# Performance work log

Measured on AMD Instinct MI355X. Metric: run time of the kernel, lower is better.

## Reference

```python
import jax, jax.numpy as jnp
import numpy as np
import math

B, N, E, H = 2, 2048, 1024, 16
D = E // H

def setup_inputs() -> dict:
    key = jax.random.key(0)
    ks = jax.random.split(key, 9)
    s = 1.0 / math.sqrt(E)
    return {
        "x": jax.random.normal(ks[0], (B, N, E), dtype=jnp.float32),
        "Wq": jax.random.uniform(ks[1], (E, E), jnp.float32, -s, s),
        "bq": jax.random.uniform(ks[2], (E,), jnp.float32, -s, s),
        "Wk": jax.random.uniform(ks[3], (E, E), jnp.float32, -s, s),
        "bk": jax.random.uniform(ks[4], (E,), jnp.float32, -s, s),
        "Wv": jax.random.uniform(ks[5], (E, E), jnp.float32, -s, s),
        "bv": jax.random.uniform(ks[6], (E,), jnp.float32, -s, s),
        "Wo": jax.random.uniform(ks[7], (E, E), jnp.float32, -s, s),
        "bo": jax.random.uniform(ks[8], (E,), jnp.float32, -s, s),
    }

def _split_heads(t):
    # [b, n, (h d)] -> [b, h, n, d]
    b, n, _ = t.shape
    return t.reshape(b, n, H, D).transpose(0, 2, 1, 3)

def reference(x, Wq, bq, Wk, bk, Wv, bv, Wo, bo):
    q = _split_heads(x @ Wq.T + bq)
    k = _split_heads(x @ Wk.T + bk)
    v = _split_heads(x @ Wv.T + bv)
    energy = jnp.einsum('bhqd,bhkd->bhqk', q, k)
    # Faithful to source: softmax first, THEN divide by sqrt(n_embedding)
    attention = jax.nn.softmax(energy, axis=-1) / jnp.sqrt(jnp.float32(E))
    out = jnp.einsum('bhqk,bhkd->bhqd', attention, v)
    out = out.transpose(0, 2, 1, 3).reshape(x.shape[0], x.shape[1], E)
    return out @ Wo.T + bo
```

## Files before the change

### kernel.cpp

```cpp
#include <hip/hip_runtime.h>


typedef __bf16 bf16x8 __attribute__((ext_vector_type(8)));
typedef float  f32x4  __attribute__((ext_vector_type(4)));
typedef float  f32x16 __attribute__((ext_vector_type(16)));
using u16 = unsigned short;
using u32 = unsigned int;
typedef u16 u16x8 __attribute__((ext_vector_type(8)));
typedef u16 u16x4 __attribute__((ext_vector_type(4)));
typedef u32 u32x4 __attribute__((ext_vector_type(4)));

constexpr int BATCH = 2, SEQ = 2048, EMB = 1024, NH = 16, HD = 64;
constexpr int MTOT = BATCH * SEQ;
constexpr int KTOT = EMB;
constexpr int NTOT = EMB;
constexpr float LOG2E = 1.44269504088896340736f;

constexpr size_t OFF_XBF = 0;
constexpr size_t OFF_WQ  = 8u * 1024 * 1024;
constexpr size_t OFF_WK  = OFF_WQ + 2u * 1024 * 1024;
constexpr size_t OFF_WV  = OFF_WK + 2u * 1024 * 1024;
constexpr size_t OFF_WO  = OFF_WV + 2u * 1024 * 1024;
constexpr size_t OFF_Q   = OFF_WO + 2u * 1024 * 1024;
constexpr size_t OFF_K   = OFF_Q  + 8u * 1024 * 1024;
constexpr size_t OFF_VT  = OFF_K  + 8u * 1024 * 1024;

__device__ __forceinline__ u16 f2bf(float f) {
  u32 u = __builtin_bit_cast(u32, f);
  u = (u + 0x7fffu + ((u >> 16) & 1u)) >> 16;
  return (u16)u;
}

__device__ __forceinline__ bf16x8 ld_bf16x8(const u16* p) {
  return __builtin_bit_cast(bf16x8, *(const u16x8*)p);
}

__device__ __forceinline__ float fexp2(float x) {
#if __has_builtin(__builtin_amdgcn_exp2f)
  return __builtin_amdgcn_exp2f(x);
#else
  return exp2f(x);
#endif
}

__device__ __forceinline__ float fmax3(float a, float b, float c) {
  float d;
  asm("v_max3_f32 %0, %1, %2, %3" : "=v"(d) : "v"(a), "v"(b), "v"(c));
  return d;
}

__device__ __forceinline__ u32 cvtpk(float lo, float hi_) {
  u32 r;
  asm("v_cvt_pk_bf16_f32 %0, %1, %2" : "=v"(r) : "v"(lo), "v"(hi_));
  return r;
}

__device__ __forceinline__ void stage16(const void* g, void* l) {
#if __has_builtin(__builtin_amdgcn_global_load_lds)
  __builtin_amdgcn_global_load_lds(
      (__attribute__((address_space(1))) void*)const_cast<void*>(g),
      (__attribute__((address_space(3))) void*)l, 16, 0, 0);
#else
  int lane = threadIdx.x & 63;
  uint4 v = *(const uint4*)g;
  *(uint4*)((char*)l + lane * 16) = v;
#endif
}

__global__ __launch_bounds__(256) void cvt_all(
    const float* __restrict__ x, const float* __restrict__ wq,
    const float* __restrict__ wk, const float* __restrict__ wv,
    const float* __restrict__ wo, u16* __restrict__ ox, u16* __restrict__ oq,
    u16* __restrict__ okk, u16* __restrict__ ov, u16* __restrict__ oo) {
  int id = blockIdx.x;
  const float* in;
  u16* out;
  int i;
  if (id < 4096) {
    in = x; out = ox; i = id * 256 + threadIdx.x;
  } else {
    int z = (id - 4096) >> 10, r = (id - 4096) & 1023;
    in = (z == 0) ? wq : (z == 1) ? wk : (z == 2) ? wv : wo;
    out = (z == 0) ? oq : (z == 1) ? okk : (z == 2) ? ov : oo;
    i = r * 256 + threadIdx.x;
  }
  float4 f = ((const float4*)in)[i];
  u32 lo = (u32)f2bf(f.x) | ((u32)f2bf(f.y) << 16);
  u32 hi = (u32)f2bf(f.z) | ((u32)f2bf(f.w) << 16);
  ((uint2*)out)[i] = make_uint2(lo, hi);
}

__device__ __forceinline__ void gemm_bt_core(const u16* __restrict__ A,
                                             const u16* __restrict__ Bm,
                                             const float* __restrict__ bias,
                                             void* __restrict__ out, int mode,
                                             float oscale) {
  __shared__ __align__(16) u16 smem[2][2][128 * 32];
  const int tid = threadIdx.x, w = tid >> 6, ln = tid & 63;
  const int wr = w >> 1, wc = w & 1, qq = ln >> 4, t = ln & 15;
  const int m0 = blockIdx.y * 128, n0 = blockIdx.x * 128;

  f32x4 acc[4][4] = {};

#define GSTAGE(bi, kt)                                                         \
  {                                                                            \
    _Pragma("unroll") for (int j = 0; j < 2; j++) {                            \
      int ck = w * 128 + j * 64 + ln;                                          \
      int r = ck >> 2, c2 = ck & 3;                                            \
      stage16(&A[(size_t)(m0 + r) * KTOT + (kt) + c2 * 8],                     \
              &smem[bi][0][(w * 128 + j * 64) * 8]);                           \
      stage16(&Bm[(size_t)(n0 + r) * KTOT + (kt) + c2 * 8],                    \
              &smem[bi][1][(w * 128 + j * 64) * 8]);                           \
    }                                                                          \
  }

  GSTAGE(0, 0)
  __syncthreads();

  int bs = 0;
  for (int kt = 0; kt < KTOT; kt += 32, bs ^= 1) {
    if (kt + 32 < KTOT) GSTAGE(bs ^ 1, kt + 32)
    const u16* sA = smem[bs][0];
    const u16* sB = smem[bs][1];

    bf16x8 av[4], bv[4];
#pragma unroll
    for (int f = 0; f < 4; f++) {
      av[f] = ld_bf16x8(&sA[(wr * 64 + f * 16 + t) * 32 + qq * 8]);
      bv[f] = ld_bf16x8(&sB[(wc * 64 + f * 16 + t) * 32 + qq * 8]);
    }
#pragma unroll
    for (int i = 0; i < 4; i++)
#pragma unroll
      for (int j = 0; j < 4; j++)
        acc[i][j] = __builtin_amdgcn_mfma_f32_16x16x32_bf16(av[i], bv[j], acc[i][j], 0, 0, 0);
    __syncthreads();
  }
#undef GSTAGE

  if (mode == 1) {
    u16* tb = (u16*)smem;
    const int b = m0 >> 11, tokb = (m0 & 2047) + t * 8;
#pragma unroll
    for (int ph = 0; ph < 2; ph++) {
      if (ph == 1) __syncthreads();
      if (wc == ph) {
#pragma unroll
        for (int fc = 0; fc < 4; fc++) {
          int nl = fc * 16 + t;
          float bn = bias[n0 + ph * 64 + nl];
#pragma unroll
          for (int fr = 0; fr < 4; fr++)
#pragma unroll
            for (int i = 0; i < 4; i++) {
              int ml = wr * 64 + fr * 16 + qq * 4 + i;
              tb[nl * 128 + (ml ^ ((nl & 7) << 4))] = f2bf(acc[fr][fc][i] + bn);
            }
        }
      }
      __syncthreads();
#pragma unroll
      for (int s = 0; s < 4; s++) {
        int row = w * 16 + s * 4 + qq;
        int n = n0 + ph * 64 + row;
        int hh = n >> 6, d = n & 63;
        u16x8 vd = *(const u16x8*)&tb[row * 128 + ((t * 8) ^ ((row & 7) << 4))];
        *(u16x8*)&((u16*)out)[(((size_t)(b * NH + hh)) * HD + d) * SEQ + tokb] = vd;
      }
    }
    return;
  }

#pragma unroll
  for (int fc = 0; fc < 4; fc++) {
    int n = n0 + wc * 64 + fc * 16 + t;
    float bn = bias[n];
#pragma unroll
    for (int fr = 0; fr < 4; fr++) {
#pragma unroll
      for (int i = 0; i < 4; i++) {
        int m = m0 + wr * 64 + fr * 16 + qq * 4 + i;
        float v = (acc[fr][fc][i] + bn) * oscale;
        if (mode == 2) {
          ((float*)out)[(size_t)m * NTOT + n] = v;
        } else {
          int b = m >> 11, tok = m & 2047, h = n >> 6, d = n & 63;
          ((u16*)out)[(((size_t)(b * NH + h)) * SEQ + tok) * HD + d] = f2bf(v);
        }
      }
    }
  }
}

__global__ __launch_bounds__(256) void gemm_qkv(
    const u16* __restrict__ A, const u16* __restrict__ WQ, const u16* __restrict__ WK,
    const u16* __restrict__ WV, const float* __restrict__ bq, const float* __restrict__ bk,
    const float* __restrict__ bv, u16* Qo, u16* Ko, u16* Vo) {
  int z = blockIdx.z;
  const u16* Bm = (z == 0) ? WQ : ((z == 1) ? WK : WV);
  const float* bias = (z == 0) ? bq : ((z == 1) ? bk : bv);
  u16* out = (z == 0) ? Qo : ((z == 1) ? Ko : Vo);
  gemm_bt_core(A, Bm, bias, out, (z == 2) ? 1 : 0, (z == 0) ? LOG2E : 1.0f);
}

__global__ __launch_bounds__(256) void gemm_o(const u16* __restrict__ A,
                                              const u16* __restrict__ WO,
                                              const float* __restrict__ bo,
                                              float* __restrict__ out) {
  gemm_bt_core(A, WO, bo, out, 2, 1.0f);
}

__global__ __launch_bounds__(512, 4) void flash_attn(const u16* __restrict__ Q,
                                                     const u16* __restrict__ Kg,
                                                     const u16* __restrict__ VT,
                                                     u16* __restrict__ O) {
  const int e = blockIdx.x;
  const int xcd = e & 7, slot = e >> 3;
  const int bh = xcd * 4 + (slot & 3);
  const int qt = slot >> 2;

  const int tid = threadIdx.x, w = tid >> 6, ln = tid & 63;
  const int c = ln & 31, hi = ln >> 5;
  const int kb = w >> 2;
  const int q0 = qt * 128 + (w & 3) * 32;

  const u16* Qb = Q + (size_t)bh * SEQ * HD;
  const u16* Kb = Kg + (size_t)bh * SEQ * HD;
  const u16* Vb = VT + (size_t)bh * HD * SEQ;

  __shared__ __align__(16) u16 sK[3][64 * 64];
  __shared__ __align__(16) u16 sV[3][64 * 64];
  __shared__ float2 sml[8][64];

  bf16x8 qf[4];
#pragma unroll
  for (int ks = 0; ks < 4; ks++)
    qf[ks] = ld_bf16x8(&Qb[(size_t)(q0 + c) * HD + ks * 16 + hi * 8]);

  const bf16x8 ones = __builtin_bit_cast(
      bf16x8, (u16x8){0x3f80, 0x3f80, 0x3f80, 0x3f80, 0x3f80, 0x3f80, 0x3f80, 0x3f80});

  f32x16 ot[2];
  ot[0] = 0.f; ot[1] = 0.f;
  f32x16 acc_l = 0.f;
  float m = -1e30f;

#define STAGE(pK, pV, kt)                                                      \
  {                                                                            \
    int ck = w * 64 + ln;                                                      \
    int r = ck >> 3, c2 = ck & 7, c2s = c2 ^ (r & 7);                          \
    stage16(&Kb[(size_t)((kt) + r) * HD + c2s * 8], (pK) + (size_t)(w * 64) * 8); \
    stage16(&Vb[(size_t)r * SEQ + (kt) + c2s * 8], (pV) + (size_t)(w * 64) * 8);  \
  }

#define QKT(stv, pK)                                                           \
  {                                                                            \
    stv = 0.f;                                                                 \
    __builtin_amdgcn_s_setprio(1);                                             \
    _Pragma("unroll") for (int ks = 0; ks < 4; ks++) {                         \
      int row = kb * 32 + c;                                                   \
      int boff = ((2 * ks + hi) ^ (row & 7)) << 4;                             \
      bf16x8 kf = ld_bf16x8((const u16*)((const char*)((pK) + row * 64) + boff)); \
      stv = __builtin_amdgcn_mfma_f32_32x32x16_bf16(kf, qf[ks], stv, 0, 0, 0); \
    }                                                                          \
    __builtin_amdgcn_s_setprio(0);                                             \
  }

#define SMAX(stv)                                                              \
  {                                                                            \
    float a0 = fmax3(stv[0], stv[1], stv[2]);                                  \
    float a1 = fmax3(stv[3], stv[4], stv[5]);                                  \
    float a2 = fmax3(stv[6], stv[7], stv[8]);                                  \
    float a3 = fmax3(stv[9], stv[10], stv[11]);                                \
    float a4 = fmax3(stv[12], stv[13], stv[14]);                               \
    float a5 = fmaxf(stv[15], a0);                                             \
    float b0 = fmax3(a1, a2, a3);                                              \
    float b1 = fmax3(a4, a5, b0);                                              \
    float pmax = fmaxf(b1, __shfl_xor(b1, 32));                                \
    if (!__all(pmax <= m + 8.0f)) {              \
      float mn = fmaxf(m, pmax);                                               \
      float sc = fexp2(m - mn);                                                \
      acc_l[0] *= sc;                                                          \
      _Pragma("unroll") for (int i = 0; i < 16; i++) {                         \
        ot[0][i] *= sc; ot[1][i] *= sc;                                        \
      }                                                                        \
      m = mn;                                                                  \
    }                                                                          \
    _Pragma("unroll") for (int i = 0; i < 16; i++) stv[i] = fexp2(stv[i] - m); \
    _Pragma("unroll") for (int ks2 = 0; ks2 < 2; ks2++) {                      \
      const int R0 = 8 * ks2;                                                  \
      const int R1 = 4 * ((2 * ks2 + 1) & 3);                                  \
      u32 X0 = cvtpk(stv[R0], stv[R0 + 1]);                                    \
      u32 X1 = cvtpk(stv[R0 + 2], stv[R0 + 3]);                                \
      u32 Y0 = cvtpk(stv[R1], stv[R1 + 1]);                                    \
      u32 Y1 = cvtpk(stv[R1 + 2], stv[R1 + 3]);                                \
      asm("v_permlane32_swap_b32 %0, %1" : "+v"(X0), "+v"(Y0));                \
      asm("v_permlane32_swap_b32 %0, %1" : "+v"(X1), "+v"(Y1));                \
      u32x4 wd; wd.x = X0; wd.y = X1; wd.z = Y0; wd.w = Y1;                    \
      pb[ks2] = __builtin_bit_cast(bf16x8, wd);                                \
    }                                                                          \
  }

#define PV(pV)                                                                 \
  {                                                                            \
    __builtin_amdgcn_s_setprio(1);                                             \
    _Pragma("unroll") for (int ks2 = 0; ks2 < 2; ks2++) {                      \
      _Pragma("unroll") for (int db = 0; db < 2; db++) {                       \
        int row = db * 32 + c;                                                 \
        int boff = ((kb * 4 + ks2 * 2 + hi) ^ (row & 7)) << 4;                 \
        bf16x8 vf = ld_bf16x8((const u16*)((const char*)((pV) + row * 64) + boff)); \
        ot[db] = __builtin_amdgcn_mfma_f32_32x32x16_bf16(vf, pb[ks2], ot[db], 0, 0, 0); \
      }                                                                        \
      acc_l = __builtin_amdgcn_mfma_f32_32x32x16_bf16(ones, pb[ks2], acc_l, 0, 0, 0); \
    }                                                                          \
    __builtin_amdgcn_s_setprio(0);                                             \
  }

#define BODY(t, SC, SN)                                                        \
  {                                                                            \
    if ((t) + 2 < 32) STAGE(kF, vF, ((t) + 2) * 64);                           \
    if ((t) + 1 < 32) QKT(SN, kN);                                             \
    bf16x8 pb[2];                                                              \
    SMAX(SC);                                                                  \
    PV(vC);                                                                    \
    __syncthreads();                                                           \
    u16* tk = kC; kC = kN; kN = kF; kF = tk;                                   \
    u16* tv = vC; vC = vN; vN = vF; vF = tv;                                   \
  }

  u16 *kC = sK[0], *kN = sK[1], *kF = sK[2];
  u16 *vC = sV[0], *vN = sV[1], *vF = sV[2];

  f32x16 stA, stB;

  STAGE(kC, vC, 0)
  __syncthreads();
  QKT(stA, kC)
  STAGE(kN, vN, 64)
  __syncthreads();

  for (int t = 0; t < 32; t += 2) {
    BODY(t, stA, stB)
    BODY(t + 1, stB, stA)
  }
#undef STAGE
#undef QKT
#undef SMAX
#undef PV
#undef BODY

  float myl = acc_l[0];
  const int pair = w & 3;
  float* xA = (float*)sK;
  float* xB = (float*)sV;
  {
    f32x16 give = (w < 4) ? ot[1] : ot[0];
    *(f32x16*)((w < 4 ? xA : xB) + (size_t)(pair * 64 + ln) * 16) = give;
    sml[w][ln] = make_float2(m, myl);
  }
  __syncthreads();

  float2 po = sml[w ^ 4][ln];
  float M2 = fmaxf(m, po.x);
  float s_me = fexp2(m - M2), s_po = fexp2(po.x - M2);
  float lf = myl * s_me + po.y * s_po;
  float inv = 1.0f / (lf * 32.0f);
  f32x16 oth = *(const f32x16*)((w < 4 ? xB : xA) + (size_t)(pair * 64 + ln) * 16);
  f32x16 own = (w < 4) ? ot[0] : ot[1];
  const int db = (w < 4) ? 0 : 1;

  const int b = bh >> 4, h = bh & 15;
  u16* obase = O + ((size_t)(b * SEQ + q0 + c)) * EMB + h * HD;
#pragma unroll
  for (int g = 0; g < 4; g++) {
    u16x4 pkt;
#pragma unroll
    for (int i = 0; i < 4; i++)
      pkt[i] = f2bf((own[g * 4 + i] * s_me + oth[g * 4 + i] * s_po) * inv);
    *(u16x4*)(obase + db * 32 + g * 8 + hi * 4) = pkt;
  }
}

extern "C" void kernel_launch(void* const* d_in, const int* in_sizes, int n_in,
                              void* d_out, int out_size, void* d_ws, size_t ws_size,
                              hipStream_t stream) {
  const float* x  = (const float*)d_in[0];
  const float* Wq = (const float*)d_in[1];
  const float* bq = (const float*)d_in[2];
  const float* Wk = (const float*)d_in[3];
  const float* bk = (const float*)d_in[4];
  const float* Wv = (const float*)d_in[5];
  const float* bv = (const float*)d_in[6];
  const float* Wo = (const float*)d_in[7];
  const float* bo = (const float*)d_in[8];

  char* ws = (char*)d_ws;
  u16* xbf = (u16*)(ws + OFF_XBF);
  u16* wqb = (u16*)(ws + OFF_WQ);
  u16* wkb = (u16*)(ws + OFF_WK);
  u16* wvb = (u16*)(ws + OFF_WV);
  u16* wob = (u16*)(ws + OFF_WO);
  u16* Qw  = (u16*)(ws + OFF_Q);
  u16* Kw  = (u16*)(ws + OFF_K);
  u16* Vw  = (u16*)(ws + OFF_VT);

  cvt_all<<<dim3(8192), 256, 0, stream>>>(x, Wq, Wk, Wv, Wo, xbf, wqb, wkb, wvb, wob);

  gemm_qkv<<<dim3(NTOT / 128, MTOT / 128, 3), 256, 0, stream>>>(
      xbf, wqb, wkb, wvb, bq, bk, bv, Qw, Kw, Vw);

  flash_attn<<<dim3(512), 512, 0, stream>>>(Qw, Kw, Vw, xbf);

  gemm_o<<<dim3(NTOT / 128, MTOT / 128), 256, 0, stream>>>(xbf, wob, bo, (float*)d_out);
}
```

Measured before the change: 134.8 us.

## Use 512-thread GEMM blocks and compute softmax row sums with shuffles

The projection GEMMs now run 512 threads per 128x128 tile, so each of the 8 waves owns a 32x64 sub-tile with half the accumulators and does one staging load instead of two. In flash attention, the row-sum l is now accumulated with VALU adds and a cross-half shuffle instead of an extra MFMA against a ones vector. The softmax and PV macros are merged and the loop body is written out inline. The GEMM change raises the thread count and lowers per-wave work and registers, at the cost of more synchronisation per block. The attention change removes one MFMA per k-step in exchange for extra VALU adds and shuffles.

Measured after the change: 115.8 us. -14.1%, faster.

```diff
diff --git a/kernel.cpp b/kernel.cpp
--- a/kernel.cpp
+++ b/kernel.cpp
@@ -100,18 +100,16 @@
   const int wr = w >> 1, wc = w & 1, qq = ln >> 4, t = ln & 15;
   const int m0 = blockIdx.y * 128, n0 = blockIdx.x * 128;
 
-  f32x4 acc[4][4] = {};
+  f32x4 acc[2][4] = {};
 
 #define GSTAGE(bi, kt)                                                         \
   {                                                                            \
-    _Pragma("unroll") for (int j = 0; j < 2; j++) {                            \
-      int ck = w * 128 + j * 64 + ln;                                          \
-      int r = ck >> 2, c2 = ck & 3;                                            \
-      stage16(&A[(size_t)(m0 + r) * KTOT + (kt) + c2 * 8],                     \
-              &smem[bi][0][(w * 128 + j * 64) * 8]);                           \
-      stage16(&Bm[(size_t)(n0 + r) * KTOT + (kt) + c2 * 8],                    \
-              &smem[bi][1][(w * 128 + j * 64) * 8]);                           \
-    }                                                                          \
+    int ck = w * 64 + ln;                                          \
+    int r = ck >> 2, c2 = ck & 3;                                              \
+    stage16(&A[(size_t)(m0 + r) * KTOT + (kt) + c2 * 8],                       \
+            &smem[bi][0][(size_t)(w * 64) * 8]);                               \
+    stage16(&Bm[(size_t)(n0 + r) * KTOT + (kt) + c2 * 8],                      \
+            &smem[bi][1][(size_t)(w * 64) * 8]);                               \
   }
 
   GSTAGE(0, 0)
@@ -123,14 +121,15 @@
     const u16* sA = smem[bs][0];
     const u16* sB = smem[bs][1];
 
-    bf16x8 av[4], bv[4];
-#pragma unroll
-    for (int f = 0; f < 4; f++) {
-      av[f] = ld_bf16x8(&sA[(wr * 64 + f * 16 + t) * 32 + qq * 8]);
+    bf16x8 av[2], bv[4];
+#pragma unroll
+    for (int f = 0; f < 2; f++)
+      av[f] = ld_bf16x8(&sA[(wr * 32 + f * 16 + t) * 32 + qq * 8]);
+#pragma unroll
+    for (int f = 0; f < 4; f++)
       bv[f] = ld_bf16x8(&sB[(wc * 64 + f * 16 + t) * 32 + qq * 8]);
-    }
-#pragma unroll
-    for (int i = 0; i < 4; i++)
+#pragma unroll
+    for (int i = 0; i < 2; i++)
 #pragma unroll
       for (int j = 0; j < 4; j++)
         acc[i][j] = __builtin_amdgcn_mfma_f32_16x16x32_bf16(av[i], bv[j], acc[i][j], 0, 0, 0);
@@ -140,7 +139,9 @@
 
   if (mode == 1) {
     u16* tb = (u16*)smem;
-    const int b = m0 >> 11, tokb = (m0 & 2047) + t * 8;
+    const int b = m0 >> 11;
+    const int t16 = tid & 15;
+    const int tokb = (m0 & 2047) + t16 * 8;
 #pragma unroll
     for (int ph = 0; ph < 2; ph++) {
       if (ph == 1) __syncthreads();
@@ -150,21 +151,21 @@
           int nl = fc * 16 + t;
           float bn = bias[n0 + ph * 64 + nl];
 #pragma unroll
-          for (int fr = 0; fr < 4; fr++)
+          for (int fr = 0; fr < 2; fr++)
 #pragma unroll
             for (int i = 0; i < 4; i++) {
-              int ml = wr * 64 + fr * 16 + qq * 4 + i;
+              int ml = wr * 32 + fr * 16 + qq * 4 + i;
               tb[nl * 128 + (ml ^ ((nl & 7) << 4))] = f2bf(acc[fr][fc][i] + bn);
             }
         }
       }
       __syncthreads();
 #pragma unroll
-      for (int s = 0; s < 4; s++) {
-        int row = w * 16 + s * 4 + qq;
+      for (int p = 0; p < 2; p++) {
+        int row = p * 32 + (tid >> 4);
         int n = n0 + ph * 64 + row;
         int hh = n >> 6, d = n & 63;
-        u16x8 vd = *(const u16x8*)&tb[row * 128 + ((t * 8) ^ ((row & 7) << 4))];
+        u16x8 vd = *(const u16x8*)&tb[row * 128 + ((t16 * 8) ^ ((row & 7) << 4))];
         *(u16x8*)&((u16*)out)[(((size_t)(b * NH + hh)) * HD + d) * SEQ + tokb] = vd;
       }
     }
@@ -176,10 +177,10 @@
     int n = n0 + wc * 64 + fc * 16 + t;
     float bn = bias[n];
 #pragma unroll
-    for (int fr = 0; fr < 4; fr++) {
+    for (int fr = 0; fr < 2; fr++) {
 #pragma unroll
       for (int i = 0; i < 4; i++) {
-        int m = m0 + wr * 64 + fr * 16 + qq * 4 + i;
+        int m = m0 + wr * 32 + fr * 16 + qq * 4 + i;
         float v = (acc[fr][fc][i] + bn) * oscale;
         if (mode == 2) {
           ((float*)out)[(size_t)m * NTOT + n] = v;
@@ -192,7 +193,7 @@
   }
 }
 
-__global__ __launch_bounds__(256) void gemm_qkv(
+__global__ __launch_bounds__(512) void gemm_qkv(
     const u16* __restrict__ A, const u16* __restrict__ WQ, const u16* __restrict__ WK,
     const u16* __restrict__ WV, const float* __restrict__ bq, const float* __restrict__ bk,
     const float* __restrict__ bv, u16* Qo, u16* Ko, u16* Vo) {
@@ -203,7 +204,7 @@
   gemm_bt_core(A, Bm, bias, out, (z == 2) ? 1 : 0, (z == 0) ? LOG2E : 1.0f);
 }
 
-__global__ __launch_bounds__(256) void gemm_o(const u16* __restrict__ A,
+__global__ __launch_bounds__(512) void gemm_o(const u16* __restrict__ A,
                                               const u16* __restrict__ WO,
                                               const float* __restrict__ bo,
                                               float* __restrict__ out) {
@@ -237,13 +238,9 @@
   for (int ks = 0; ks < 4; ks++)
     qf[ks] = ld_bf16x8(&Qb[(size_t)(q0 + c) * HD + ks * 16 + hi * 8]);
 
-  const bf16x8 ones = __builtin_bit_cast(
-      bf16x8, (u16x8){0x3f80, 0x3f80, 0x3f80, 0x3f80, 0x3f80, 0x3f80, 0x3f80, 0x3f80});
-
   f32x16 ot[2];
   ot[0] = 0.f; ot[1] = 0.f;
-  f32x16 acc_l = 0.f;
-  float m = -1e30f;
+  float m = -1e30f, l = 0.f;
 
 #define STAGE(pK, pV, kt)                                                      \
   {                                                                            \
@@ -266,7 +263,7 @@
     __builtin_amdgcn_s_setprio(0);                                             \
   }
 
-#define SMAX(stv)                                                              \
+#define SMAXPV(stv, pV)                                                        \
   {                                                                            \
     float a0 = fmax3(stv[0], stv[1], stv[2]);                                  \
     float a1 = fmax3(stv[3], stv[4], stv[5]);                                  \
@@ -280,13 +277,20 @@
     if (!__all(pmax <= m + 8.0f)) {              \
       float mn = fmaxf(m, pmax);                                               \
       float sc = fexp2(m - mn);                                                \
-      acc_l[0] *= sc;                                                          \
+      l *= sc;                                                                 \
       _Pragma("unroll") for (int i = 0; i < 16; i++) {                         \
         ot[0][i] *= sc; ot[1][i] *= sc;                                        \
       }                                                                        \
       m = mn;                                                                  \
     }                                                                          \
     _Pragma("unroll") for (int i = 0; i < 16; i++) stv[i] = fexp2(stv[i] - m); \
+    float u0 = (stv[0] + stv[1]) + (stv[2] + stv[3]);                          \
+    float u1 = (stv[4] + stv[5]) + (stv[6] + stv[7]);                          \
+    float u2 = (stv[8] + stv[9]) + (stv[10] + stv[11]);                        \
+    float u3 = (stv[12] + stv[13]) + (stv[14] + stv[15]);                      \
+    float rs = (u0 + u1) + (u2 + u3);                                          \
+    l += rs + __shfl_xor(rs, 32);                                              \
+    bf16x8 pb[2];                                                              \
     _Pragma("unroll") for (int ks2 = 0; ks2 < 2; ks2++) {                      \
       const int R0 = 8 * ks2;                                                  \
       const int R1 = 4 * ((2 * ks2 + 1) & 3);                                  \
@@ -299,10 +303,6 @@
       u32x4 wd; wd.x = X0; wd.y = X1; wd.z = Y0; wd.w = Y1;                    \
       pb[ks2] = __builtin_bit_cast(bf16x8, wd);                                \
     }                                                                          \
-  }
-
-#define PV(pV)                                                                 \
-  {                                                                            \
     __builtin_amdgcn_s_setprio(1);                                             \
     _Pragma("unroll") for (int ks2 = 0; ks2 < 2; ks2++) {                      \
       _Pragma("unroll") for (int db = 0; db < 2; db++) {                       \
@@ -311,22 +311,13 @@
         bf16x8 vf = ld_bf16x8((const u16*)((const char*)((pV) + row * 64) + boff)); \
         ot[db] = __builtin_amdgcn_mfma_f32_32x32x16_bf16(vf, pb[ks2], ot[db], 0, 0, 0); \
       }                                                                        \
-      acc_l = __builtin_amdgcn_mfma_f32_32x32x16_bf16(ones, pb[ks2], acc_l, 0, 0, 0); \
     }                                                                          \
     __builtin_amdgcn_s_setprio(0);                                             \
   }
 
-#define BODY(t, SC, SN)                                                        \
-  {                                                                            \
-    if ((t) + 2 < 32) STAGE(kF, vF, ((t) + 2) * 64);                           \
-    if ((t) + 1 < 32) QKT(SN, kN);                                             \
-    bf16x8 pb[2];                                                              \
-    SMAX(SC);                                                                  \
-    PV(vC);                                                                    \
-    __syncthreads();                                                           \
-    u16* tk = kC; kC = kN; kN = kF; kF = tk;                                   \
-    u16* tv = vC; vC = vN; vN = vF; vF = tv;                                   \
-  }
+#define ROTATE()                                                               \
+  { u16* x_ = kC; kC = kN; kN = kF; kF = x_;                                   \
+    x_ = vC; vC = vN; vN = vF; vF = x_; }
 
   u16 *kC = sK[0], *kN = sK[1], *kF = sK[2];
   u16 *vC = sV[0], *vN = sV[1], *vF = sV[2];
@@ -340,16 +331,23 @@
   __syncthreads();
 
   for (int t = 0; t < 32; t += 2) {
-    BODY(t, stA, stB)
-    BODY(t + 1, stB, stA)
+    if (t + 2 < 32) STAGE(kF, vF, (t + 2) * 64)
+    if (t + 1 < 32) QKT(stB, kN)
+    SMAXPV(stA, vC)
+    __syncthreads();
+    ROTATE()
+    if (t + 3 < 32) STAGE(kF, vF, (t + 3) * 64)
+    if (t + 2 < 32) QKT(stA, kN)
+    SMAXPV(stB, vC)
+    __syncthreads();
+    ROTATE()
   }
 #undef STAGE
 #undef QKT
-#undef SMAX
-#undef PV
-#undef BODY
-
-  float myl = acc_l[0];
+#undef SMAXPV
+#undef ROTATE
+
+  float myl = l;
   const int pair = w & 3;
   float* xA = (float*)sK;
   float* xB = (float*)sV;
@@ -406,10 +404,10 @@
 
   cvt_all<<<dim3(8192), 256, 0, stream>>>(x, Wq, Wk, Wv, Wo, xbf, wqb, wkb, wvb, wob);
 
-  gemm_qkv<<<dim3(NTOT / 128, MTOT / 128, 3), 256, 0, stream>>>(
+  gemm_qkv<<<dim3(NTOT / 128, MTOT / 128, 3), 512, 0, stream>>>(
       xbf, wqb, wkb, wvb, bq, bk, bv, Qw, Kw, Vw);
 
   flash_attn<<<dim3(512), 512, 0, stream>>>(Qw, Kw, Vw, xbf);
 
-  gemm_o<<<dim3(NTOT / 128, MTOT / 128), 256, 0, stream>>>(xbf, wob, bo, (float*)d_out);
-}
+  gemm_o<<<dim3(NTOT / 128, MTOT / 128), 512, 0, stream>>>(xbf, wob, bo, (float*)d_out);
+}
```
